# Kernel optimization log

Hardware: AMD Instinct MI355X
Metric: run time of the kernel (lower is better)

Reference implementation:

```python
import jax, jax.numpy as jnp
import numpy as np

# Config (matches init_kwargs)
N, P, K, DIMS = 16, 1024, 16, 3
C_IN, C_MID, C_OUT, DM = 64, 64, 128, 4
C_CAT = C_MID + C_IN          # channels entering depthwise-separable conv
KK = K * K
BN_EPS = 1e-5


def setup_inputs() -> dict:
    key = jax.random.key(0)
    ks = jax.random.split(key, 24)
    s = 0.05  # small init scale for weights
    inp = {
        # forward args
        "rep_pt": jax.random.normal(ks[0], (N, P, DIMS), jnp.float32),
        "pts":    jax.random.normal(ks[1], (N, P, K, DIMS), jnp.float32),
        "fts":    jax.random.normal(ks[2], (N, P, K, C_IN), jnp.float32),
        # dense1 / dense2 (point lifting MLP), weights stored (in, out)
        "w1": jax.random.normal(ks[3], (DIMS, C_MID), jnp.float32) * s,
        "b1": jnp.zeros((C_MID,), jnp.float32),
        "w2": jax.random.normal(ks[4], (C_MID, C_MID), jnp.float32) * s,
        "b2": jnp.zeros((C_MID,), jnp.float32),
        # conv1: Conv2d(dims, K*K, (1,K)); weight (KK, dims, K)
        "wc1": jax.random.normal(ks[5], (KK, DIMS, K), jnp.float32) * s,
        "bc1": jnp.zeros((KK,), jnp.float32),
        # x_dense1 (ELU) and x_dense2 (no activation)
        "wx1": jax.random.normal(ks[6], (KK, KK), jnp.float32) * s,
        "bx1": jnp.zeros((KK,), jnp.float32),
        "wx2": jax.random.normal(ks[7], (KK, KK), jnp.float32) * s,
        "bx2": jnp.zeros((KK,), jnp.float32),
        # depthwise Conv2d(C_CAT, C_CAT*DM, (1,K), groups=C_CAT): weight (C_CAT, DM, K)
        "wdw": jax.random.normal(ks[8], (C_CAT, DM, K), jnp.float32) * s,
        "bdw": jnp.zeros((C_CAT * DM,), jnp.float32),
        # pointwise Conv2d(C_CAT*DM, C_OUT, 1): weight stored (C_CAT*DM, C_OUT)
        "wpw": jax.random.normal(ks[9], (C_CAT * DM, C_OUT), jnp.float32) * s,
        "bpw": jnp.zeros((C_OUT,), jnp.float32),
        # BatchNorm2d(C_OUT) in eval mode (running stats)
        "bn_gamma": jnp.ones((C_OUT,), jnp.float32),
        "bn_beta":  jnp.zeros((C_OUT,), jnp.float32),
        "bn_mean":  jax.random.normal(ks[10], (C_OUT,), jnp.float32) * 0.1,
        "bn_var":   jax.random.uniform(ks[11], (C_OUT,), jnp.float32, 0.5, 1.5),
    }
    return inp


def reference(rep_pt, pts, fts, w1, b1, w2, b2, wc1, bc1, wx1, bx1, wx2, bx2,
              wdw, bdw, wpw, bpw, bn_gamma, bn_beta, bn_mean, bn_var):
    elu = jax.nn.elu
    n, p, k = pts.shape[0], pts.shape[1], pts.shape[2]

    # localize points around representative point: (N,P,K,dims)
    pts_local = pts - rep_pt[:, :, None, :]

    # lift coordinates to C_mid features (two Dense+ELU)
    h = elu(pts_local @ w1 + b1)
    h = elu(h @ w2 + b2)
    fts_cat = jnp.concatenate([h, fts], axis=-1)  # (N,P,K,C_CAT)

    # learned X-transform: conv1 over the K neighbors -> (N,P,K*K)
    X = elu(jnp.einsum('npkd,odk->npo', pts_local, wc1) + bc1)
    X = elu(X @ wx1 + bx1)
    X = X @ wx2 + bx2            # x_dense2: no activation
    X = X.reshape(n, p, k, k)    # (N,P,K,K)

    # apply X-transform to concatenated features
    fts_X = jnp.einsum('npij,npjc->npic', X, fts_cat)  # (N,P,K,C_CAT)

    # depthwise conv (kernel (1,K), groups=C_CAT, depth multiplier DM)
    # torch grouped-conv channel order: out channel o = c*DM + d
    dw = jnp.einsum('npkc,cdk->npcd', fts_X, wdw).reshape(n, p, -1) + bdw
    # pointwise 1x1 conv -> C_OUT, then ELU
    y = elu(dw @ wpw + bpw)      # (N,P,C_OUT)
    # BatchNorm2d in eval mode (per-channel affine with running stats)
    y = (y - bn_mean) * (bn_gamma / jnp.sqrt(bn_var + BN_EPS)) + bn_beta
    return y                     # (N,P,C_OUT)
```

## Files before the change

kernel.cpp:

```cpp
#include <hip/hip_runtime.h>

#define NPTS 16384
#define MPB  16
#define NTHR 512
#define WS_NEEDED 401408u

typedef __attribute__((ext_vector_type(8))) short bf16x8;
typedef __attribute__((ext_vector_type(4))) float f32x4;

__device__ __forceinline__ unsigned short f2bf(float x) {
    unsigned u = __float_as_uint(x);
    return (unsigned short)((u + 0x7FFFu + ((u >> 16) & 1u)) >> 16);
}
__device__ __forceinline__ unsigned pk2(float a, float b) {
    return (unsigned)f2bf(a) | ((unsigned)f2bf(b) << 16);
}
__device__ __forceinline__ float bf2f(unsigned short h) {
    return __uint_as_float(((unsigned)h) << 16);
}
__device__ __forceinline__ float elu_f(float x) {
    return x > 0.f ? x : (__expf(x) - 1.f);
}

__device__ __forceinline__ bf16x8 load_bfrag(const float* __restrict__ W, int N,
                                             int kt, int nt, int lane) {
    int k0  = kt * 32 + ((lane >> 4) << 3);
    int col = nt * 16 + (lane & 15);
    const float* s = W + k0 * N + col;
    bf16x8 r;
#pragma unroll
    for (int j = 0; j < 8; j++) r[j] = (short)f2bf(s[j * N]);
    return r;
}

__global__ void pack_weights(const float* __restrict__ w2,
                             const float* __restrict__ wx1,
                             const float* __restrict__ wx2,
                             const float* __restrict__ wpw,
                             unsigned short* __restrict__ dst) {
    int gid  = blockIdx.x * 256 + threadIdx.x;
    int frag = gid >> 6, lane = gid & 63;
    const float* src; int N, fl;
    if      (frag <   8) { src = w2;  N =  64; fl = frag;       }
    else if (frag < 136) { src = wx1; N = 256; fl = frag - 8;   }
    else if (frag < 264) { src = wx2; N = 256; fl = frag - 136; }
    else                 { src = wpw; N = 128; fl = frag - 264; }
    int NT  = N >> 4;
    int kt  = fl / NT, nt = fl - kt * NT;
    int k0  = kt * 32 + (lane >> 4) * 8;
    int col = nt * 16 + (lane & 15);
    const float* s = src + k0 * N + col;
    unsigned v[4];
#pragma unroll
    for (int u = 0; u < 4; u++) {
        unsigned lo = f2bf(s[(2 * u) * N]);
        unsigned hi = f2bf(s[(2 * u + 1) * N]);
        v[u] = lo | (hi << 16);
    }
    *(uint4*)&dst[gid * 8] = make_uint4(v[0], v[1], v[2], v[3]);
}

template <bool PACKED>
__global__ __launch_bounds__(NTHR, 4)
void xconv_main(const float* __restrict__ rep_pt, const float* __restrict__ pts,
                const float* __restrict__ fts,
                const float* __restrict__ w1,  const float* __restrict__ b1,
                const float* __restrict__ w2,  const float* __restrict__ b2,
                const float* __restrict__ wc1, const float* __restrict__ bc1,
                const float* __restrict__ wx1, const float* __restrict__ bx1,
                const float* __restrict__ wx2, const float* __restrict__ bx2,
                const float* __restrict__ wdw, const float* __restrict__ bdw,
                const float* __restrict__ wpw, const float* __restrict__ bpw,
                const float* __restrict__ bn_gamma, const float* __restrict__ bn_beta,
                const float* __restrict__ bn_mean,  const float* __restrict__ bn_var,
                const unsigned short* __restrict__ wpack,
                float* __restrict__ out) {
    __shared__ __align__(16) char smem[60928];
    float*          s_ptsl = (float*)smem;
    unsigned short* s_h2f  = (unsigned short*)(smem + 3072);
    unsigned short* s_h1   = (unsigned short*)(smem + 35840);
    unsigned short* s_x0   = (unsigned short*)(smem + 35840);
    unsigned short* s_x2f  = (unsigned short*)(smem + 35840);
    unsigned short* s_x1   = (unsigned short*)(smem + 44288);
    unsigned short* s_dw   = (unsigned short*)(smem + 44288);

    const int t    = threadIdx.x;
    const int lane = t & 63;
    const int w    = t >> 6;
    const int cl   = lane & 15;
    const int hh   = lane >> 4;
    const int gp0  = blockIdx.x * MPB;

    for (int idx = t; idx < MPB * 48; idx += NTHR) {
        int m = idx / 48, r = idx - m * 48;
        int k = r / 3,    d = r - k * 3;
        int gp = gp0 + m;
        s_ptsl[idx] = pts[(gp * 16 + k) * 3 + d] - rep_pt[gp * 3 + d];
    }
    __syncthreads();

    {
        const bf16x8* wp = (const bf16x8*)wpack;
        bf16x8 Bf[8];
#pragma unroll
        for (int f = 0; f < 8; f++) {
            if (PACKED) Bf[f] = wp[f * 64 + lane];
            else        Bf[f] = load_bfrag(w2, 64, f >> 2, f & 3, lane);
        }
        float bias[4];
#pragma unroll
        for (int nt = 0; nt < 4; nt++) bias[nt] = b2[nt * 16 + cl];

        for (int R = 0; R < 2; R++) {
            if (t < 256) {
                int lr  = t >> 1;
                int row = 128 * R + lr;
                int m = row >> 4, k = row & 15;
                float p0 = s_ptsl[m * 48 + k * 3 + 0];
                float p1 = s_ptsl[m * 48 + k * 3 + 1];
                float p2 = s_ptsl[m * 48 + k * 3 + 2];
                int cb = (t & 1) * 32;
#pragma unroll
                for (int cc = 0; cc < 4; cc++) {
                    unsigned v[4];
#pragma unroll
                    for (int u = 0; u < 4; u++) {
                        int c0 = cb + cc * 8 + u * 2;
                        float a  = fmaf(p0, w1[c0],     fmaf(p1, w1[64 + c0],     fmaf(p2, w1[128 + c0],     b1[c0])));
                        float bb = fmaf(p0, w1[c0 + 1], fmaf(p1, w1[64 + c0 + 1], fmaf(p2, w1[128 + c0 + 1], b1[c0 + 1])));
                        v[u] = pk2(elu_f(a), elu_f(bb));
                    }
                    *(uint4*)&s_h1[lr * 72 + cb + cc * 8] = make_uint4(v[0], v[1], v[2], v[3]);
                }
            }
            __syncthreads();
            {
                int rtl = w;
                int m   = 8 * R + rtl;
                bf16x8 a0 = *(const bf16x8*)&s_h1[(rtl * 16 + cl) * 72 + 0  + hh * 8];
                bf16x8 a1 = *(const bf16x8*)&s_h1[(rtl * 16 + cl) * 72 + 32 + hh * 8];
#pragma unroll
                for (int nt = 0; nt < 4; nt++) {
                    f32x4 acc = {bias[nt], bias[nt], bias[nt], bias[nt]};
                    acc = __builtin_amdgcn_mfma_f32_16x16x32_bf16(a0, Bf[0 * 4 + nt], acc, 0, 0, 0);
                    acc = __builtin_amdgcn_mfma_f32_16x16x32_bf16(a1, Bf[1 * 4 + nt], acc, 0, 0, 0);
                    unsigned lo = pk2(elu_f(acc[0]), elu_f(acc[1]));
                    unsigned hi = pk2(elu_f(acc[2]), elu_f(acc[3]));
                    unsigned short* dp = &s_h2f[(((m * 4 + nt) * 32) + (hh >> 1) * 16 + cl) * 8 + (hh & 1) * 4];
                    *(uint2*)dp = make_uint2(lo, hi);
                }
            }
            __syncthreads();
        }
    }

    {
        const int o     = t & 255;
        const int mbase = (t >> 8) * 8;
        float wreg[48];
#pragma unroll
        for (int q = 0; q < 12; q++) {
            float4 wv = *(const float4*)&wc1[o * 48 + q * 4];
            wreg[q * 4 + 0] = wv.x; wreg[q * 4 + 1] = wv.y;
            wreg[q * 4 + 2] = wv.z; wreg[q * 4 + 3] = wv.w;
        }
        float bo = bc1[o];
#pragma unroll 1
        for (int ml = 0; ml < 8; ml++) {
            int m = mbase + ml;
            float acc = bo;
#pragma unroll
            for (int q = 0; q < 12; q++) {
                float4 pv = *(const float4*)&s_ptsl[m * 48 + q * 4];
                acc = fmaf(pv.x, wreg[((q * 4 + 0) % 3) * 16 + (q * 4 + 0) / 3], acc);
                acc = fmaf(pv.y, wreg[((q * 4 + 1) % 3) * 16 + (q * 4 + 1) / 3], acc);
                acc = fmaf(pv.z, wreg[((q * 4 + 2) % 3) * 16 + (q * 4 + 2) / 3], acc);
                acc = fmaf(pv.w, wreg[((q * 4 + 3) % 3) * 16 + (q * 4 + 3) / 3], acc);
            }
            s_x0[m * 264 + o] = f2bf(elu_f(acc));
        }
    }
    __syncthreads();

    {
        const bf16x8* wp = (const bf16x8*)wpack + 512;
        f32x4 acc[2];
#pragma unroll
        for (int q = 0; q < 2; q++) {
            float bv = bx1[(w * 2 + q) * 16 + cl];
            acc[q] = (f32x4){bv, bv, bv, bv};
        }
#pragma unroll
        for (int kt = 0; kt < 8; kt++) {
            bf16x8 a = *(const bf16x8*)&s_x0[cl * 264 + kt * 32 + hh * 8];
#pragma unroll
            for (int q = 0; q < 2; q++) {
                int nt = w * 2 + q;
                bf16x8 b;
                if (PACKED) b = wp[(kt * 16 + nt) * 64 + lane];
                else        b = load_bfrag(wx1, 256, kt, nt, lane);
                acc[q] = __builtin_amdgcn_mfma_f32_16x16x32_bf16(a, b, acc[q], 0, 0, 0);
            }
        }
#pragma unroll
        for (int q = 0; q < 2; q++) {
            int nt = w * 2 + q;
#pragma unroll
            for (int r = 0; r < 4; r++) {
                int m = hh * 4 + r;
                s_x1[m * 264 + nt * 16 + cl] = f2bf(elu_f(acc[q][r]));
            }
        }
    }
    __syncthreads();

    {
        const bf16x8* wp = (const bf16x8*)wpack + 8704;
        f32x4 acc[2];
#pragma unroll
        for (int q = 0; q < 2; q++) {
            float bv = bx2[(w * 2 + q) * 16 + cl];
            acc[q] = (f32x4){bv, bv, bv, bv};
        }
#pragma unroll
        for (int kt = 0; kt < 8; kt++) {
            bf16x8 a = *(const bf16x8*)&s_x1[cl * 264 + kt * 32 + hh * 8];
#pragma unroll
            for (int q = 0; q < 2; q++) {
                int nt = w * 2 + q;
                bf16x8 b;
                if (PACKED) b = wp[(kt * 16 + nt) * 64 + lane];
                else        b = load_bfrag(wx2, 256, kt, nt, lane);
                acc[q] = __builtin_amdgcn_mfma_f32_16x16x32_bf16(a, b, acc[q], 0, 0, 0);
            }
        }
#pragma unroll
        for (int q = 0; q < 2; q++) {
            int ntE = w * 2 + q;
            int lp  = (cl >> 3) * 16 + ntE;
            int jj  = cl & 7;
#pragma unroll
            for (int r = 0; r < 4; r++) {
                int m = hh * 4 + r;
                s_x2f[(m * 32 + lp) * 8 + jj] = f2bf(acc[q][r]);
            }
        }
    }
    __syncthreads();

    {
        const int  cH    = (w & 3) * 16 + cl;
        const bool isF   = (w >= 4);
        const int  cFull = isF ? (64 + cH) : cH;
        float wd[16];
#pragma unroll
        for (int d = 0; d < 4; d++) {
            float4 v = *(const float4*)&wdw[cFull * 64 + d * 16 + 4 * hh];
            wd[d * 4 + 0] = v.x; wd[d * 4 + 1] = v.y;
            wd[d * 4 + 2] = v.z; wd[d * 4 + 3] = v.w;
        }
        float4 bd = *(const float4*)&bdw[cFull * 4];
        const float* ftsp = fts + (size_t)gp0 * 1024 + cH;

        float f0[8], f1[8];
        auto LDF = [&](int m, float* f) {
            if (isF && lane < 32) {
                const float* p = ftsp + (m * 16 + hh * 8) * 64;
#pragma unroll
                for (int j = 0; j < 8; j++) f[j] = p[j * 64];
            }
        };
        auto BODY = [&](int m, float* fc_, float* fn_) {
            if (m < 15) LDF(m + 1, fn_);
            bf16x8 a = {};
            if (lane < 32) a = *(const bf16x8*)&s_x2f[(m * 32 + lane) * 8];
            bf16x8 b = {};
            if (isF) {
                if (lane < 32) {
                    union { bf16x8 v; uint4 u; } ub;
                    ub.u = make_uint4(pk2(fc_[0], fc_[1]), pk2(fc_[2], fc_[3]),
                                      pk2(fc_[4], fc_[5]), pk2(fc_[6], fc_[7]));
                    b = ub.v;
                }
            } else {
                if (lane < 32) b = *(const bf16x8*)&s_h2f[((m * 4 + (w & 3)) * 32 + lane) * 8];
            }
            f32x4 acc = {0.f, 0.f, 0.f, 0.f};
            acc = __builtin_amdgcn_mfma_f32_16x16x32_bf16(a, b, acc, 0, 0, 0);
            float o[4];
#pragma unroll
            for (int d = 0; d < 4; d++) {
                float s = acc[0] * wd[d * 4 + 0];
                s = fmaf(acc[1], wd[d * 4 + 1], s);
                s = fmaf(acc[2], wd[d * 4 + 2], s);
                s = fmaf(acc[3], wd[d * 4 + 3], s);
                s += __shfl_xor(s, 16);
                s += __shfl_xor(s, 32);
                o[d] = s;
            }
            if (hh == 0) {
                ushort4 v;
                v.x = f2bf(o[0] + bd.x); v.y = f2bf(o[1] + bd.y);
                v.z = f2bf(o[2] + bd.z); v.w = f2bf(o[3] + bd.w);
                *(ushort4*)&s_dw[m * 520 + cFull * 4] = v;
            }
        };
        LDF(0, f0);
#pragma unroll
        for (int mm = 0; mm < 8; mm++) {
            BODY(2 * mm + 0, f0, f1);
            BODY(2 * mm + 1, f1, f0);
        }
    }
    __syncthreads();

    {
        const bf16x8* wp = (const bf16x8*)wpack + 16896;
        float bv = bpw[w * 16 + cl];
        f32x4 acc = {bv, bv, bv, bv};
#pragma unroll
        for (int kt = 0; kt < 16; kt++) {
            bf16x8 a = *(const bf16x8*)&s_dw[cl * 520 + kt * 32 + hh * 8];
            bf16x8 b;
            if (PACKED) b = wp[(kt * 8 + w) * 64 + lane];
            else        b = load_bfrag(wpw, 128, kt, w, lane);
            acc = __builtin_amdgcn_mfma_f32_16x16x32_bf16(a, b, acc, 0, 0, 0);
        }
        int co = w * 16 + cl;
        float scale = bn_gamma[co] * rsqrtf(bn_var[co] + 1e-5f);
        float shift = bn_beta[co] - bn_mean[co] * scale;
#pragma unroll
        for (int r = 0; r < 4; r++) {
            int m = hh * 4 + r;
            out[(gp0 + m) * 128 + co] = fmaf(elu_f(acc[r]), scale, shift);
        }
    }
}

extern "C" void kernel_launch(void* const* d_in, const int* in_sizes, int n_in,
                              void* d_out, int out_size, void* d_ws, size_t ws_size,
                              hipStream_t stream) {
    const float* rep_pt   = (const float*)d_in[0];
    const float* pts      = (const float*)d_in[1];
    const float* fts      = (const float*)d_in[2];
    const float* w1       = (const float*)d_in[3];
    const float* b1       = (const float*)d_in[4];
    const float* w2       = (const float*)d_in[5];
    const float* b2       = (const float*)d_in[6];
    const float* wc1      = (const float*)d_in[7];
    const float* bc1      = (const float*)d_in[8];
    const float* wx1      = (const float*)d_in[9];
    const float* bx1      = (const float*)d_in[10];
    const float* wx2      = (const float*)d_in[11];
    const float* bx2      = (const float*)d_in[12];
    const float* wdw      = (const float*)d_in[13];
    const float* bdw      = (const float*)d_in[14];
    const float* wpw      = (const float*)d_in[15];
    const float* bpw      = (const float*)d_in[16];
    const float* bn_gamma = (const float*)d_in[17];
    const float* bn_beta  = (const float*)d_in[18];
    const float* bn_mean  = (const float*)d_in[19];
    const float* bn_var   = (const float*)d_in[20];
    float* out = (float*)d_out;

    const bool packed = (d_ws != nullptr) && (ws_size >= (size_t)WS_NEEDED);
    unsigned short* wpack = (unsigned short*)d_ws;

    if (packed) {
        pack_weights<<<98, 256, 0, stream>>>(w2, wx1, wx2, wpw, wpack);
        xconv_main<true><<<NPTS / MPB, NTHR, 0, stream>>>(
            rep_pt, pts, fts, w1, b1, w2, b2, wc1, bc1, wx1, bx1, wx2, bx2,
            wdw, bdw, wpw, bpw, bn_gamma, bn_beta, bn_mean, bn_var, wpack, out);
    } else {
        xconv_main<false><<<NPTS / MPB, NTHR, 0, stream>>>(
            rep_pt, pts, fts, w1, b1, w2, b2, wc1, bc1, wx1, bx1, wx2, bx2,
            wdw, bdw, wpw, bpw, bn_gamma, bn_beta, bn_mean, bn_var, (const unsigned short*)nullptr, out);
    }
}
```

Measured before the change: 200.9 us.

## Split warps between lifting MLP and conv1, build dense1 fragments in registers

Warps 4-7 now compute the dense1 layer straight into MFMA A-fragments in registers and run dense2 on 4 tiles each, so the s_h1 staging buffer and two __syncthreads per round go away. Warps 0-3 run the conv1 X-transform over all 16 points at the same time. This is meant to overlap the two independent stages and cut barriers and LDS traffic. In exchange, each lifting warp now handles four tiles and holds more weights in registers, so register pressure rises, and the two warp groups are uneven in work.

```diff
diff --git a/kernel.cpp b/kernel.cpp
--- a/kernel.cpp
+++ b/kernel.cpp
@@ -78,7 +78,6 @@
     __shared__ __align__(16) char smem[60928];
     float*          s_ptsl = (float*)smem;
     unsigned short* s_h2f  = (unsigned short*)(smem + 3072);
-    unsigned short* s_h1   = (unsigned short*)(smem + 35840);
     unsigned short* s_x0   = (unsigned short*)(smem + 35840);
     unsigned short* s_x2f  = (unsigned short*)(smem + 35840);
     unsigned short* s_x1   = (unsigned short*)(smem + 44288);
@@ -99,7 +98,7 @@
     }
     __syncthreads();
 
-    {
+    if (w >= 4) {
         const bf16x8* wp = (const bf16x8*)wpack;
         bf16x8 Bf[8];
 #pragma unroll
@@ -110,64 +109,64 @@
         float bias[4];
 #pragma unroll
         for (int nt = 0; nt < 4; nt++) bias[nt] = b2[nt * 16 + cl];
-
-        for (int R = 0; R < 2; R++) {
-            if (t < 256) {
-                int lr  = t >> 1;
-                int row = 128 * R + lr;
-                int m = row >> 4, k = row & 15;
-                float p0 = s_ptsl[m * 48 + k * 3 + 0];
-                float p1 = s_ptsl[m * 48 + k * 3 + 1];
-                float p2 = s_ptsl[m * 48 + k * 3 + 2];
-                int cb = (t & 1) * 32;
-#pragma unroll
-                for (int cc = 0; cc < 4; cc++) {
-                    unsigned v[4];
-#pragma unroll
-                    for (int u = 0; u < 4; u++) {
-                        int c0 = cb + cc * 8 + u * 2;
-                        float a  = fmaf(p0, w1[c0],     fmaf(p1, w1[64 + c0],     fmaf(p2, w1[128 + c0],     b1[c0])));
-                        float bb = fmaf(p0, w1[c0 + 1], fmaf(p1, w1[64 + c0 + 1], fmaf(p2, w1[128 + c0 + 1], b1[c0 + 1])));
-                        v[u] = pk2(elu_f(a), elu_f(bb));
-                    }
-                    *(uint4*)&s_h1[lr * 72 + cb + cc * 8] = make_uint4(v[0], v[1], v[2], v[3]);
+        float w1s[2][3][8], b1s[2][8];
+#pragma unroll
+        for (int kt = 0; kt < 2; kt++) {
+#pragma unroll
+            for (int d = 0; d < 3; d++)
+#pragma unroll
+                for (int j = 0; j < 8; j++)
+                    w1s[kt][d][j] = w1[d * 64 + kt * 32 + hh * 8 + j];
+#pragma unroll
+            for (int j = 0; j < 8; j++) b1s[kt][j] = b1[kt * 32 + hh * 8 + j];
+        }
+#pragma unroll
+        for (int i = 0; i < 4; i++) {
+            int tile = (w - 4) * 4 + i;
+            float p0 = s_ptsl[tile * 48 + cl * 3 + 0];
+            float p1 = s_ptsl[tile * 48 + cl * 3 + 1];
+            float p2 = s_ptsl[tile * 48 + cl * 3 + 2];
+            bf16x8 a[2];
+#pragma unroll
+            for (int kt = 0; kt < 2; kt++) {
+                unsigned v[4];
+#pragma unroll
+                for (int u = 0; u < 4; u++) {
+                    int j0 = 2 * u, j1 = 2 * u + 1;
+                    float ha = elu_f(fmaf(p0, w1s[kt][0][j0],
+                                     fmaf(p1, w1s[kt][1][j0],
+                                     fmaf(p2, w1s[kt][2][j0], b1s[kt][j0]))));
+                    float hb = elu_f(fmaf(p0, w1s[kt][0][j1],
+                                     fmaf(p1, w1s[kt][1][j1],
+                                     fmaf(p2, w1s[kt][2][j1], b1s[kt][j1]))));
+                    v[u] = pk2(ha, hb);
                 }
-            }
-            __syncthreads();
-            {
-                int rtl = w;
-                int m   = 8 * R + rtl;
-                bf16x8 a0 = *(const bf16x8*)&s_h1[(rtl * 16 + cl) * 72 + 0  + hh * 8];
-                bf16x8 a1 = *(const bf16x8*)&s_h1[(rtl * 16 + cl) * 72 + 32 + hh * 8];
-#pragma unroll
-                for (int nt = 0; nt < 4; nt++) {
-                    f32x4 acc = {bias[nt], bias[nt], bias[nt], bias[nt]};
-                    acc = __builtin_amdgcn_mfma_f32_16x16x32_bf16(a0, Bf[0 * 4 + nt], acc, 0, 0, 0);
-                    acc = __builtin_amdgcn_mfma_f32_16x16x32_bf16(a1, Bf[1 * 4 + nt], acc, 0, 0, 0);
-                    unsigned lo = pk2(elu_f(acc[0]), elu_f(acc[1]));
-                    unsigned hi = pk2(elu_f(acc[2]), elu_f(acc[3]));
-                    unsigned short* dp = &s_h2f[(((m * 4 + nt) * 32) + (hh >> 1) * 16 + cl) * 8 + (hh & 1) * 4];
-                    *(uint2*)dp = make_uint2(lo, hi);
-                }
-            }
-            __syncthreads();
-        }
-    }
-
-    {
-        const int o     = t & 255;
-        const int mbase = (t >> 8) * 8;
+                union { bf16x8 b8; uint4 u4; } ua;
+                ua.u4 = make_uint4(v[0], v[1], v[2], v[3]);
+                a[kt] = ua.b8;
+            }
+#pragma unroll
+            for (int nt = 0; nt < 4; nt++) {
+                f32x4 acc = {bias[nt], bias[nt], bias[nt], bias[nt]};
+                acc = __builtin_amdgcn_mfma_f32_16x16x32_bf16(a[0], Bf[0 * 4 + nt], acc, 0, 0, 0);
+                acc = __builtin_amdgcn_mfma_f32_16x16x32_bf16(a[1], Bf[1 * 4 + nt], acc, 0, 0, 0);
+                unsigned lo = pk2(elu_f(acc[0]), elu_f(acc[1]));
+                unsigned hi = pk2(elu_f(acc[2]), elu_f(acc[3]));
+                unsigned short* dp = &s_h2f[(((tile * 4 + nt) * 32) + (hh >> 1) * 16 + cl) * 8 + (hh & 1) * 4];
+                *(uint2*)dp = make_uint2(lo, hi);
+            }
+        }
+    } else {
         float wreg[48];
 #pragma unroll
         for (int q = 0; q < 12; q++) {
-            float4 wv = *(const float4*)&wc1[o * 48 + q * 4];
+            float4 wv = *(const float4*)&wc1[t * 48 + q * 4];
             wreg[q * 4 + 0] = wv.x; wreg[q * 4 + 1] = wv.y;
             wreg[q * 4 + 2] = wv.z; wreg[q * 4 + 3] = wv.w;
         }
-        float bo = bc1[o];
+        float bo = bc1[t];
 #pragma unroll 1
-        for (int ml = 0; ml < 8; ml++) {
-            int m = mbase + ml;
+        for (int m = 0; m < MPB; m++) {
             float acc = bo;
 #pragma unroll
             for (int q = 0; q < 12; q++) {
@@ -177,7 +176,7 @@
                 acc = fmaf(pv.z, wreg[((q * 4 + 2) % 3) * 16 + (q * 4 + 2) / 3], acc);
                 acc = fmaf(pv.w, wreg[((q * 4 + 3) % 3) * 16 + (q * 4 + 3) / 3], acc);
             }
-            s_x0[m * 264 + o] = f2bf(elu_f(acc));
+            s_x0[m * 264 + t] = f2bf(elu_f(acc));
         }
     }
     __syncthreads();
```

Measured after the change: 219.0 us. 1.09x slower.
